# Performance work log

Measured on AMD Instinct MI355X. Metric: run time of the kernel, lower is better.

Reference implementation:

```python
import jax, jax.numpy as jnp
import numpy as np

B, G, D, E = 16, 2048, 2048, 32          # batch, genes, drug fp dim, gene embed dim
NL, NM, H, GS = 16, 4, 6, 64             # n leaves, n mids, term hidden, genes per leaf
GAMMA, NDRUG, EPS = 0.5, 1024, 1e-5

def _bn3(x):  # BatchNorm1d on [B, C, L], training stats, affine at init (gamma=1, beta=0)
    m = x.mean(axis=(0, 2), keepdims=True)
    v = x.var(axis=(0, 2), keepdims=True)
    return (x - m) / jnp.sqrt(v + EPS)

def _bn2(x):  # BatchNorm1d on [B, C]
    m = x.mean(axis=0, keepdims=True)
    v = x.var(axis=0, keepdims=True)
    return (x - m) / jnp.sqrt(v + EPS)

def _term(ci, W1, b1, Wc, bc, Wd, bd):
    # ci: [B, E, in] child input; returns ([B,H,E] 3d out, [B,H] 2d out)
    h = jnp.einsum('bei,hi->bhe', ci, W1) + b1[None, :, None]      # linear -> permute
    h = _bn3(h)
    c = jnp.einsum('bhe,kh->bke', h, Wc) + bc[None, :, None]       # context layer
    out3d = _bn3(c)                                                # [B,H,E]
    mean = out3d.mean(axis=1)                                      # [B,E]
    out2d = _bn2(jnp.tanh(mean @ Wd.T + bd))                       # dimension layer
    return out3d, out2d

def setup_inputs():
    key = jax.random.key(0)
    ks = iter(jax.random.split(key, 64))
    def rn(shape):
        return jax.random.normal(next(ks), shape, dtype=jnp.float32) * 0.05
    x = jax.random.normal(next(ks), (B, G + D + 1), dtype=jnp.float32)
    idx = jax.random.randint(next(ks), (B,), 0, NDRUG)
    x = x.at[:, -1].set(idx.astype(jnp.float32))
    table = jax.random.randint(next(ks), (NDRUG, G), 0, G, dtype=jnp.int32)
    inp = dict(x=x, table=table,
        W_rbf=rn((E, G)), b_rbf=rn((E,)), emb=rn((G, E)),
        W_dg=rn((NL, GS, G)), b_dg=rn((NL, GS)),
        Wl1=rn((NL, H, GS)), bl1=rn((NL, H)), Wlc=rn((NL, H, H)), blc=rn((NL, H)),
        Wld=rn((NL, H, E)), bld=rn((NL, H)),
        Wm1=rn((NM, H, 4 * H)), bm1=rn((NM, H)), Wmc=rn((NM, H, H)), bmc=rn((NM, H)),
        Wmd=rn((NM, H, E)), bmd=rn((NM, H)),
        Wr1=rn((H, 4 * H)), br1=rn((H,)), Wrc=rn((H, H)), brc=rn((H,)),
        Wrd=rn((H, E)), brd=rn((H,)),
        Wd1=rn((100, D)), bd1=rn((100,)), Wd2=rn((50, 100)), bd2=rn((50,)),
        Wd3=rn((H, 50)), bd3=rn((H,)),
        Wf=rn((6, 2 * H)), bf=rn((6,)), Wfa=rn((1, 6)), bfa=rn((1,)),
        Wfo=rn((1, 1)), bfo=rn((1,)))
    return inp

def reference(x, W_rbf, b_rbf, emb, W_dg, b_dg,
              Wl1, bl1, Wlc, blc, Wld, bld,
              Wm1, bm1, Wmc, bmc, Wmd, bmd,
              Wr1, br1, Wrc, brc, Wrd, brd,
              Wd1, bd1, Wd2, bd2, Wd3, bd3,
              Wf, bf, Wfa, bfa, Wfo, bfo, table):
    g = x[:, :G]
    drug = x[:, G:G + D]
    idx = x[:, G + D].astype(jnp.int32)
    # RBF kernel: [B, G, G]
    vect = jnp.exp(-GAMMA * jnp.square(g[:, :, None] - g[:, None, :]))
    gv = jnp.einsum('bij,ej->bie', vect, W_rbf) + b_rbf            # [B,G,E]
    lv = emb[table[idx]]                                            # [B,G,E]
    gf = (gv + lv).transpose(0, 2, 1)                               # [B,E,G]
    # per-leaf direct gene layers
    gene_out = jnp.einsum('beg,lkg->lbek', gf, W_dg) + b_dg[:, None, None, :]  # [NL,B,E,GS]
    leaf3d, _ = jax.vmap(_term)(gene_out, Wl1, bl1, Wlc, blc, Wld, bld)        # [NL,B,H,E]
    # mid terms: concat 4 leaf children along feature dim
    a = leaf3d.transpose(0, 1, 3, 2).reshape(NM, 4, B, E, H)
    a = jnp.moveaxis(a, 1, 3).reshape(NM, B, E, 4 * H)
    mid3d, _ = jax.vmap(_term)(a, Wm1, bm1, Wmc, bmc, Wmd, bmd)                # [NM,B,H,E]
    r = jnp.moveaxis(mid3d.transpose(0, 1, 3, 2), 0, 2).reshape(B, E, 4 * H)
    _, root2d = _term(r, Wr1, br1, Wrc, brc, Wrd, brd)                          # [B,H]
    # drug MLP
    d = drug
    for Wl, bl in ((Wd1, bd1), (Wd2, bd2), (Wd3, bd3)):
        d = _bn2(jnp.tanh(d @ Wl.T + bl))
    fin = jnp.concatenate([root2d, d], axis=1)                                  # [B,2H]
    out = _bn2(jnp.tanh(fin @ Wf.T + bf))
    aux = jnp.tanh(out @ Wfa.T + bfa)
    return aux @ Wfo.T + bfo                                                    # [B,1]
```

## Files before the change

kernel.cpp:

```cpp
#include <hip/hip_runtime.h>
#include <hip/hip_bf16.h>

#define Bb 16
#define Gg 2048
#define Dd 2048
#define XS 4097
#define EPSf 1e-5f
#define CEXP (-0.72134752044448170368f)

typedef unsigned int u32;
typedef __attribute__((ext_vector_type(8))) short bf16x8;
typedef __attribute__((ext_vector_type(4))) float f32x4;

union U16 { uint4 u; bf16x8 v; };

__device__ inline float fast_exp2(float x) {
#if __has_builtin(__builtin_amdgcn_exp2f)
  return __builtin_amdgcn_exp2f(x);
#else
  return exp2f(x);
#endif
}

__device__ inline u32 pk2(float a, float b) {
  return __builtin_amdgcn_perm(__float_as_uint(b), __float_as_uint(a), 0x07060302u);
}
__device__ inline float bftrunc(float a) {
  return __uint_as_float(__float_as_uint(a) & 0xFFFF0000u);
}

__device__ inline void split8(const float* f, U16& hi, U16& lo) {
  u32 h[4], l[4];
  #pragma unroll
  for (int p = 0; p < 4; ++p) {
    float a = f[2 * p], b = f[2 * p + 1];
    h[p] = pk2(a, b);
    l[p] = pk2(a - bftrunc(a), b - bftrunc(b));
  }
  hi.u = make_uint4(h[0], h[1], h[2], h[3]);
  lo.u = make_uint4(l[0], l[1], l[2], l[3]);
}

__device__ inline float wred(float v) {
  #pragma unroll
  for (int o = 32; o > 0; o >>= 1) v += __shfl_xor(v, o, 64);
  return v;
}

__global__ __launch_bounds__(256) void k_split(const float* __restrict__ Wrbf,
                                               const float* __restrict__ Wdg,
                                               u32* __restrict__ Rhi, u32* __restrict__ Rlo,
                                               u32* __restrict__ Dhi, u32* __restrict__ Dlo) {
  int c = blockIdx.x * 256 + threadIdx.x;
  const float* src;
  u32 *dhi, *dlo;
  if (c < 8192) {
    int h = c >> 12, ks = (c >> 6) & 63, l = c & 63;
    src = Wrbf + (h * 16 + (l & 15)) * Gg + ks * 32 + (l >> 4) * 8;
    dhi = Rhi + (size_t)c * 4; dlo = Rlo + (size_t)c * 4;
  } else {
    int cc = c - 8192;
    int nf = cc >> 12, ks = (cc >> 6) & 63, l = cc & 63;
    src = Wdg + (size_t)(nf * 16 + (l & 15)) * Gg + ks * 32 + (l >> 4) * 8;
    dhi = Dhi + (size_t)cc * 4; dlo = Dlo + (size_t)cc * 4;
  }
  float4 f0 = *(const float4*)src;
  float4 f1 = *(const float4*)(src + 4);
  float f[8] = {f0.x, f0.y, f0.z, f0.w, f1.x, f1.y, f1.z, f1.w};
  U16 hi, lo;
  split8(f, hi, lo);
  *(uint4*)dhi = hi.u;
  *(uint4*)dlo = lo.u;
}

__global__ __launch_bounds__(512) void k_rbf(const float* __restrict__ x,
                                             const u32* __restrict__ Whi,
                                             const u32* __restrict__ Wlo,
                                             float4* __restrict__ partR) {
  __shared__ float g_s[512];
  __shared__ u32 w_s[8192];
  const int tid = threadIdx.x;
  const int lane = tid & 63, wid = tid >> 6;
  const int it = blockIdx.x, b = blockIdx.y, jc = blockIdx.z;
  const int i0w = it * 128 + wid * 16;
  g_s[tid] = x[(size_t)b * XS + jc * 512 + tid];
  const float gi = x[(size_t)b * XS + i0w + (lane & 15)];
  f32x4 acc0 = {0.f, 0.f, 0.f, 0.f};
  f32x4 acc1 = {0.f, 0.f, 0.f, 0.f};
  const int jb = (lane >> 4) * 8;
  const int ksbase = jc * 16;

  uint4 pf[4];
  #pragma unroll
  for (int sg = 0; sg < 4; ++sg) {
    int seg = wid * 4 + sg;
    int arr = seg >> 4, h = (seg >> 3) & 1, ksl = seg & 7;
    pf[sg] = *(const uint4*)((arr ? Wlo : Whi) +
             (((size_t)h * 64 + ksbase + ksl) * 64 + lane) * 4);
  }
  for (int chunk = 0; chunk < 2; ++chunk) {
    __syncthreads();
    #pragma unroll
    for (int sg = 0; sg < 4; ++sg)
      *(uint4*)&w_s[(wid * 4 + sg) * 256 + lane * 4] = pf[sg];
    if (chunk < 1) {
      #pragma unroll
      for (int sg = 0; sg < 4; ++sg) {
        int seg = wid * 4 + sg;
        int arr = seg >> 4, h = (seg >> 3) & 1, ksl = seg & 7;
        pf[sg] = *(const uint4*)((arr ? Wlo : Whi) +
                 (((size_t)h * 64 + ksbase + 8 + ksl) * 64 + lane) * 4);
      }
    }
    __syncthreads();
    #pragma unroll
    for (int ksl = 0; ksl < 8; ++ksl) {
      const float* gp = &g_s[chunk * 256 + ksl * 32 + jb];
      float4 gja = *(const float4*)gp;
      float4 gjb = *(const float4*)(gp + 4);
      float gv[8] = {gja.x, gja.y, gja.z, gja.w, gjb.x, gjb.y, gjb.z, gjb.w};
      float kv[8];
      #pragma unroll
      for (int q = 0; q < 8; ++q) {
        float d = gi - gv[q];
        kv[q] = fast_exp2(d * d * CEXP);
      }
      U16 ah, al;
      split8(kv, ah, al);
      U16 w0h, w1h, w0l, w1l;
      w0h.u = *(const uint4*)&w_s[(ksl) * 256 + lane * 4];
      w1h.u = *(const uint4*)&w_s[(8 + ksl) * 256 + lane * 4];
      w0l.u = *(const uint4*)&w_s[(16 + ksl) * 256 + lane * 4];
      w1l.u = *(const uint4*)&w_s[(24 + ksl) * 256 + lane * 4];
      acc0 = __builtin_amdgcn_mfma_f32_16x16x32_bf16(ah.v, w0h.v, acc0, 0, 0, 0);
      acc0 = __builtin_amdgcn_mfma_f32_16x16x32_bf16(al.v, w0h.v, acc0, 0, 0, 0);
      acc0 = __builtin_amdgcn_mfma_f32_16x16x32_bf16(ah.v, w0l.v, acc0, 0, 0, 0);
      acc1 = __builtin_amdgcn_mfma_f32_16x16x32_bf16(ah.v, w1h.v, acc1, 0, 0, 0);
      acc1 = __builtin_amdgcn_mfma_f32_16x16x32_bf16(al.v, w1h.v, acc1, 0, 0, 0);
      acc1 = __builtin_amdgcn_mfma_f32_16x16x32_bf16(ah.v, w1l.v, acc1, 0, 0, 0);
    }
  }
  size_t pbase = (((((size_t)jc * 16 + b) * 16 + it) * 8 + wid) * 2) * 64 + lane;
  partR[pbase]      = make_float4(acc0[0], acc0[1], acc0[2], acc0[3]);
  partR[pbase + 64] = make_float4(acc1[0], acc1[1], acc1[2], acc1[3]);
}

__global__ __launch_bounds__(256) void k_pack(const float4* __restrict__ partR,
                                              const float* __restrict__ x,
                                              const int* __restrict__ table,
                                              const float* __restrict__ emb,
                                              const float* __restrict__ brbf,
                                              u32* __restrict__ Ahi,
                                              u32* __restrict__ Alo) {
  int u = blockIdx.x * 256 + threadIdx.x;
  int lane = u & 63, hb = (u >> 6) & 1, wid = (u >> 7) & 7;
  int it = (u >> 10) & 15, b = u >> 14;
  float4 p0 = partR[u];
  float4 p1 = partR[262144 + u];
  float4 p2 = partR[524288 + u];
  float4 p3 = partR[786432 + u];
  int eloc = lane & 15, quad = lane >> 4;
  int e = hb * 16 + eloc;
  int i0w = it * 128 + wid * 16;
  int ib = i0w + quad * 4;
  int idx = (int)x[(size_t)b * XS + Gg + Dd];
  int4 tt = *(const int4*)&table[(size_t)idx * Gg + ib];
  float bias = brbf[e];
  float v0 = p0.x + p1.x + p2.x + p3.x + bias + emb[tt.x * 32 + e];
  float v1 = p0.y + p1.y + p2.y + p3.y + bias + emb[tt.y * 32 + e];
  float v2 = p0.z + p1.z + p2.z + p3.z + bias + emb[tt.z * 32 + e];
  float v3 = p0.w + p1.w + p2.w + p3.w + bias + emb[tt.w * 32 + e];
  int ks = i0w >> 5;
  int lp = (2 * ((i0w >> 4) & 1) + (quad >> 1)) * 16 + eloc;
  int hs = quad & 1;
  size_t off = (((size_t)(b * 2 + hb) * 64 + ks) * 64 + lp) * 4 + hs * 2;
  Ahi[off]     = pk2(v0, v1);
  Ahi[off + 1] = pk2(v2, v3);
  Alo[off]     = pk2(v0 - bftrunc(v0), v1 - bftrunc(v1));
  Alo[off + 1] = pk2(v2 - bftrunc(v2), v3 - bftrunc(v3));
}

__global__ __launch_bounds__(512) void k_mm(const u32* __restrict__ Ahi,
                                            const u32* __restrict__ Alo,
                                            const u32* __restrict__ Bhi,
                                            const u32* __restrict__ Blo,
                                            float* __restrict__ part) {
  __shared__ u32 s_mm[6144];
  const int tid = threadIdx.x;
  const int lane = tid & 63, wid = tid >> 6;
  const int id = blockIdx.x;
  const int pl = id & 7, by = (id >> 3) & 7, ph = id >> 6;
  const int p = ph * 8 + pl;
  const int bx = p >> 2, kc = p & 3;
  const int wm = wid >> 2, wn = wid & 3;
  f32x4 acc[2][2];
  #pragma unroll
  for (int mf = 0; mf < 2; ++mf)
    #pragma unroll
    for (int nf = 0; nf < 2; ++nf) acc[mf][nf] = (f32x4){0.f, 0.f, 0.f, 0.f};

  uint4 pf[3];
  #pragma unroll
  for (int q = 0; q < 3; ++q) {
    int seg = wid * 3 + q;
    const u32* src;
    if (seg < 8) {
      int hl = seg >> 2, mf = seg & 3;
      src = (hl ? Alo : Ahi) + (((size_t)(by * 4 + mf) * 64 + kc * 16) * 64 + lane) * 4;
    } else {
      int t = seg - 8, hl = t >> 3, nf = t & 7;
      src = (hl ? Blo : Bhi) + (((size_t)(bx * 8 + nf) * 64 + kc * 16) * 64 + lane) * 4;
    }
    pf[q] = *(const uint4*)src;
  }
  for (int stage = 0; stage < 16; ++stage) {
    __syncthreads();
    #pragma unroll
    for (int q = 0; q < 3; ++q)
      *(uint4*)&s_mm[(wid * 3 + q) * 256 + lane * 4] = pf[q];
    if (stage < 15) {
      const int ks = kc * 16 + stage + 1;
      #pragma unroll
      for (int q = 0; q < 3; ++q) {
        int seg = wid * 3 + q;
        const u32* src;
        if (seg < 8) {
          int hl = seg >> 2, mf = seg & 3;
          src = (hl ? Alo : Ahi) + (((size_t)(by * 4 + mf) * 64 + ks) * 64 + lane) * 4;
        } else {
          int t = seg - 8, hl = t >> 3, nf = t & 7;
          src = (hl ? Blo : Bhi) + (((size_t)(bx * 8 + nf) * 64 + ks) * 64 + lane) * 4;
        }
        pf[q] = *(const uint4*)src;
      }
    }
    __syncthreads();
    U16 ah[2], al[2], bh[2], bl[2];
    #pragma unroll
    for (int mf = 0; mf < 2; ++mf) {
      ah[mf].u = *(const uint4*)&s_mm[(0 + wm * 2 + mf) * 256 + lane * 4];
      al[mf].u = *(const uint4*)&s_mm[(4 + wm * 2 + mf) * 256 + lane * 4];
    }
    #pragma unroll
    for (int nf = 0; nf < 2; ++nf) {
      bh[nf].u = *(const uint4*)&s_mm[(8 + wn * 2 + nf) * 256 + lane * 4];
      bl[nf].u = *(const uint4*)&s_mm[(16 + wn * 2 + nf) * 256 + lane * 4];
    }
    #pragma unroll
    for (int mf = 0; mf < 2; ++mf) {
      #pragma unroll
      for (int nf = 0; nf < 2; ++nf) {
        acc[mf][nf] = __builtin_amdgcn_mfma_f32_16x16x32_bf16(ah[mf].v, bh[nf].v, acc[mf][nf], 0, 0, 0);
        acc[mf][nf] = __builtin_amdgcn_mfma_f32_16x16x32_bf16(al[mf].v, bh[nf].v, acc[mf][nf], 0, 0, 0);
        acc[mf][nf] = __builtin_amdgcn_mfma_f32_16x16x32_bf16(ah[mf].v, bl[nf].v, acc[mf][nf], 0, 0, 0);
      }
    }
  }
  const int quad = lane >> 4, nl = lane & 15;
  #pragma unroll
  for (int mf = 0; mf < 2; ++mf) {
    #pragma unroll
    for (int nf = 0; nf < 2; ++nf) {
      int n  = bx * 128 + wn * 32 + nf * 16 + nl;
      int m0 = by * 64 + wm * 32 + mf * 16 + quad * 4;
      float4 st = make_float4(acc[mf][nf][0], acc[mf][nf][1], acc[mf][nf][2], acc[mf][nf][3]);
      *(float4*)&part[(size_t)kc * 524288 + (size_t)n * 512 + m0] = st;
    }
  }
}

__device__ inline void bn512(float* v, int wv, int lane,
                             float (*r1)[6], float (*r2)[6]) {
  float s[6], q[6];
  #pragma unroll
  for (int c = 0; c < 6; ++c) {
    float a = v[c];
    s[c] = wred(a);
    q[c] = wred(a * a);
  }
  __syncthreads();
  if (lane == 0) {
    #pragma unroll
    for (int c = 0; c < 6; ++c) { r1[wv][c] = s[c]; r2[wv][c] = q[c]; }
  }
  __syncthreads();
  #pragma unroll
  for (int c = 0; c < 6; ++c) {
    float S = 0.f, Q = 0.f;
    #pragma unroll
    for (int w = 0; w < 8; ++w) { S += r1[w][c]; Q += r2[w][c]; }
    float m  = S * (1.0f / 512.0f);
    float va = Q * (1.0f / 512.0f) - m * m;
    v[c] = (v[c] - m) * rsqrtf(va + EPSf);
  }
}

__global__ __launch_bounds__(512) void k_leaf(const float* __restrict__ part,
                                              const float* __restrict__ bdg,
                                              const float* __restrict__ W1,
                                              const float* __restrict__ b1,
                                              const float* __restrict__ Wc,
                                              const float* __restrict__ bc,
                                              float* __restrict__ outp) {
  const int l = blockIdx.x, tid = threadIdx.x;
  const int wv = tid >> 6, lane = tid & 63;
  __shared__ float r1[8][6], r2[8][6];
  float cv[64];
  #pragma unroll
  for (int i = 0; i < 64; ++i) {
    int n = l * 64 + i;
    const float* pp = part + (size_t)n * 512 + tid;
    cv[i] = pp[0] + pp[524288] + pp[2 * 524288] + pp[3 * 524288] + bdg[n];
  }
  const float* w1 = W1 + l * 6 * 64;
  float h[6];
  #pragma unroll
  for (int hh = 0; hh < 6; ++hh) {
    float s = b1[l * 6 + hh];
    #pragma unroll
    for (int i = 0; i < 64; ++i) s = fmaf(cv[i], w1[hh * 64 + i], s);
    h[hh] = s;
  }
  bn512(h, wv, lane, r1, r2);
  float c[6];
  #pragma unroll
  for (int k = 0; k < 6; ++k) {
    float s = bc[l * 6 + k];
    #pragma unroll
    for (int hh = 0; hh < 6; ++hh) s = fmaf(h[hh], Wc[l * 36 + k * 6 + hh], s);
    c[k] = s;
  }
  bn512(c, wv, lane, r1, r2);
  float* o = outp + (((size_t)(l >> 2) * 512 + tid) * 24 + (l & 3) * 6);
  #pragma unroll
  for (int k = 0; k < 6; ++k) o[k] = c[k];
}

__global__ __launch_bounds__(512) void k_mid(const float* __restrict__ gin,
                                             const float* __restrict__ W1,
                                             const float* __restrict__ b1,
                                             const float* __restrict__ Wc,
                                             const float* __restrict__ bc,
                                             float* __restrict__ outp) {
  const int l = blockIdx.x, tid = threadIdx.x;
  const int wv = tid >> 6, lane = tid & 63;
  __shared__ float r1[8][6], r2[8][6];
  const float* ci = gin + ((size_t)l * 512 + tid) * 24;
  float cv[24];
  #pragma unroll
  for (int q = 0; q < 6; ++q) *(float4*)&cv[q * 4] = ((const float4*)ci)[q];
  const float* w1 = W1 + l * 6 * 24;
  float h[6];
  #pragma unroll
  for (int hh = 0; hh < 6; ++hh) {
    float s = b1[l * 6 + hh];
    #pragma unroll
    for (int i = 0; i < 24; ++i) s = fmaf(cv[i], w1[hh * 24 + i], s);
    h[hh] = s;
  }
  bn512(h, wv, lane, r1, r2);
  float c[6];
  #pragma unroll
  for (int k = 0; k < 6; ++k) {
    float s = bc[l * 6 + k];
    #pragma unroll
    for (int hh = 0; hh < 6; ++hh) s = fmaf(h[hh], Wc[l * 36 + k * 6 + hh], s);
    c[k] = s;
  }
  bn512(c, wv, lane, r1, r2);
  float* o = outp + ((size_t)tid * 24 + l * 6);
  #pragma unroll
  for (int k = 0; k < 6; ++k) o[k] = c[k];
}

__global__ __launch_bounds__(1024) void k_drug1(const float* __restrict__ x,
                                                const float* __restrict__ Wd1,
                                                const float* __restrict__ bd1,
                                                float* __restrict__ d1) {
  const int c = blockIdx.x;
  const int tid = threadIdx.x;
  const int b = tid >> 6, lane = tid & 63;
  const float* xb = x + (size_t)b * XS + Gg;
  const float* w = Wd1 + (size_t)c * 2048;
  float s = 0.f;
  #pragma unroll
  for (int q = 0; q < 8; ++q) {
    int k = q * 256 + lane * 4;
    float4 xv = *(const float4*)(xb + k);
    float4 wv = *(const float4*)(w + k);
    s = fmaf(xv.x, wv.x, s);
    s = fmaf(xv.y, wv.y, s);
    s = fmaf(xv.z, wv.z, s);
    s = fmaf(xv.w, wv.w, s);
  }
  s = wred(s);
  __shared__ float y[16];
  if (lane == 0) y[b] = tanhf(s + bd1[c]);
  __syncthreads();
  if (tid < 16) {
    float S = 0.f, Q = 0.f;
    #pragma unroll
    for (int bb = 0; bb < 16; ++bb) { float v = y[bb]; S += v; Q += v * v; }
    float m = S * (1.0f / 16.0f), va = Q * (1.0f / 16.0f) - m * m;
    d1[tid * 100 + c] = (y[tid] - m) * rsqrtf(va + EPSf);
  }
}

__global__ __launch_bounds__(512) void k_rootfinal(const float* __restrict__ rootin,
                                                   const float* __restrict__ d1,
                                                   const float* __restrict__ Wr1,
                                                   const float* __restrict__ br1,
                                                   const float* __restrict__ Wrc,
                                                   const float* __restrict__ brc,
                                                   const float* __restrict__ Wrd,
                                                   const float* __restrict__ brd,
                                                   const float* __restrict__ Wd2,
                                                   const float* __restrict__ bd2,
                                                   const float* __restrict__ Wd3,
                                                   const float* __restrict__ bd3,
                                                   const float* __restrict__ Wf,
                                                   const float* __restrict__ bf,
                                                   const float* __restrict__ Wfa,
                                                   const float* __restrict__ bfa,
                                                   const float* __restrict__ Wfo,
                                                   const float* __restrict__ bfo,
                                                   float* __restrict__ out) {
  const int tid = threadIdx.x;
  const int wv = tid >> 6, lane = tid & 63;
  __shared__ float r1[8][6], r2[8][6];
  __shared__ float w2s[50 * 101];
  __shared__ float d1s[1600];
  __shared__ float r2ds[96];
  for (int u = tid; u < 5000; u += 512) w2s[(u / 100) * 101 + (u % 100)] = Wd2[u];
  for (int u = tid; u < 1600; u += 512) d1s[u] = d1[u];

  const float* ci = rootin + (size_t)tid * 24;
  float cv[24];
  #pragma unroll
  for (int q = 0; q < 6; ++q) *(float4*)&cv[q * 4] = ((const float4*)ci)[q];
  float h[6];
  #pragma unroll
  for (int hh = 0; hh < 6; ++hh) {
    float s = br1[hh];
    #pragma unroll
    for (int i = 0; i < 24; ++i) s = fmaf(cv[i], Wr1[hh * 24 + i], s);
    h[hh] = s;
  }
  bn512(h, wv, lane, r1, r2);
  float c[6];
  #pragma unroll
  for (int k = 0; k < 6; ++k) {
    float s = brc[k];
    #pragma unroll
    for (int hh = 0; hh < 6; ++hh) s = fmaf(h[hh], Wrc[k * 6 + hh], s);
    c[k] = s;
  }
  bn512(c, wv, lane, r1, r2);
  float mv = (c[0] + c[1] + c[2] + c[3] + c[4] + c[5]) * (1.0f / 6.0f);
  __shared__ float shm[512];
  shm[tid] = mv;
  __syncthreads();
  __shared__ float st[96];
  if (tid < 96) {
    int b = tid / 6, hh = tid % 6;
    float s = brd[hh];
    #pragma unroll
    for (int e = 0; e < 32; ++e) s = fmaf(shm[b * 32 + e], Wrd[hh * 32 + e], s);
    st[tid] = tanhf(s);
  }
  __syncthreads();
  if (tid < 6) {
    float S = 0.f, Q = 0.f;
    for (int b = 0; b < 16; ++b) { float v = st[b * 6 + tid]; S += v; Q += v * v; }
    float m = S * (1.0f / 16.0f), va = Q * (1.0f / 16.0f) - m * m;
    float iv = rsqrtf(va + EPSf);
    for (int b = 0; b < 16; ++b) r2ds[b * 6 + tid] = (st[b * 6 + tid] - m) * iv;
  }
  __syncthreads();

  __shared__ float s2[800], mu2[50], iv2[50];
  for (int u = tid; u < 800; u += 512) {
    int b = u / 50, cc = u % 50;
    float s = bd2[cc];
    #pragma unroll
    for (int k = 0; k < 100; ++k) s = fmaf(d1s[b * 100 + k], w2s[cc * 101 + k], s);
    s2[u] = tanhf(s);
  }
  __syncthreads();
  if (tid < 50) {
    float S = 0.f, Q = 0.f;
    #pragma unroll
    for (int b = 0; b < 16; ++b) { float v = s2[b * 50 + tid]; S += v; Q += v * v; }
    float m = S * (1.0f / 16.0f), va = Q * (1.0f / 16.0f) - m * m;
    mu2[tid] = m; iv2[tid] = rsqrtf(va + EPSf);
  }
  __syncthreads();
  __shared__ float s3[96], mu3[6], iv3[6];
  if (tid < 96) {
    int b = tid / 6, cc = tid % 6;
    float s = bd3[cc];
    #pragma unroll
    for (int k = 0; k < 50; ++k)
      s = fmaf((s2[b * 50 + k] - mu2[k]) * iv2[k], Wd3[cc * 50 + k], s);
    s3[tid] = tanhf(s);
  }
  __syncthreads();
  if (tid < 6) {
    float S = 0.f, Q = 0.f;
    #pragma unroll
    for (int b = 0; b < 16; ++b) { float v = s3[b * 6 + tid]; S += v; Q += v * v; }
    float m = S * (1.0f / 16.0f), va = Q * (1.0f / 16.0f) - m * m;
    mu3[tid] = m; iv3[tid] = rsqrtf(va + EPSf);
  }
  __syncthreads();
  __shared__ float sf[96], muf[6], ivf[6];
  if (tid < 96) {
    int b = tid / 6, cc = tid % 6;
    float s = bf[cc];
    #pragma unroll
    for (int q = 0; q < 6; ++q) s = fmaf(r2ds[b * 6 + q], Wf[cc * 12 + q], s);
    #pragma unroll
    for (int q = 0; q < 6; ++q)
      s = fmaf((s3[b * 6 + q] - mu3[q]) * iv3[q], Wf[cc * 12 + 6 + q], s);
    sf[tid] = tanhf(s);
  }
  __syncthreads();
  if (tid < 6) {
    float S = 0.f, Q = 0.f;
    #pragma unroll
    for (int b = 0; b < 16; ++b) { float v = sf[b * 6 + tid]; S += v; Q += v * v; }
    float m = S * (1.0f / 16.0f), va = Q * (1.0f / 16.0f) - m * m;
    muf[tid] = m; ivf[tid] = rsqrtf(va + EPSf);
  }
  __syncthreads();
  if (tid < 16) {
    float s = bfa[0];
    #pragma unroll
    for (int q = 0; q < 6; ++q)
      s = fmaf((sf[tid * 6 + q] - muf[q]) * ivf[q], Wfa[q], s);
    float a = tanhf(s);
    out[tid] = a * Wfo[0] + bfo[0];
  }
}

extern "C" void kernel_launch(void* const* d_in, const int* in_sizes, int n_in,
                              void* d_out, int out_size, void* d_ws, size_t ws_size,
                              hipStream_t stream) {
  const float* x     = (const float*)d_in[0];
  const int*   table = (const int*)d_in[1];
  const float* Wrbf  = (const float*)d_in[2];
  const float* brbf  = (const float*)d_in[3];
  const float* emb   = (const float*)d_in[4];
  const float* Wdg   = (const float*)d_in[5];
  const float* bdg   = (const float*)d_in[6];
  const float* Wl1   = (const float*)d_in[7];
  const float* bl1   = (const float*)d_in[8];
  const float* Wlc   = (const float*)d_in[9];
  const float* blc   = (const float*)d_in[10];
  const float* Wm1   = (const float*)d_in[13];
  const float* bm1   = (const float*)d_in[14];
  const float* Wmc   = (const float*)d_in[15];
  const float* bmc   = (const float*)d_in[16];
  const float* Wr1   = (const float*)d_in[19];
  const float* br1   = (const float*)d_in[20];
  const float* Wrc   = (const float*)d_in[21];
  const float* brc   = (const float*)d_in[22];
  const float* Wrd   = (const float*)d_in[23];
  const float* brd   = (const float*)d_in[24];
  const float* Wd1   = (const float*)d_in[25];
  const float* bd1   = (const float*)d_in[26];
  const float* Wd2   = (const float*)d_in[27];
  const float* bd2   = (const float*)d_in[28];
  const float* Wd3   = (const float*)d_in[29];
  const float* bd3   = (const float*)d_in[30];
  const float* Wf    = (const float*)d_in[31];
  const float* bf    = (const float*)d_in[32];
  const float* Wfa   = (const float*)d_in[33];
  const float* bfa   = (const float*)d_in[34];
  const float* Wfo   = (const float*)d_in[35];
  const float* bfo   = (const float*)d_in[36];
  float* out = (float*)d_out;

  u32* Rhi = (u32*)d_ws;
  u32* Rlo = Rhi + 32768;
  u32* Dhi = Rlo + 32768;
  u32* Dlo = Dhi + 1048576;
  u32* Ahi = Dlo + 1048576;
  u32* Alo = Ahi + 524288;
  float4* partR = (float4*)(Alo + 524288);
  float* partB = (float*)(partR + 1048576);
  float* midin = partB + 4 * 524288;
  float* rootin= midin + 49152;
  float* d1    = rootin + 12288;

  hipLaunchKernelGGL(k_drug1,     dim3(100),       dim3(1024), 0, stream, x, Wd1, bd1, d1);
  hipLaunchKernelGGL(k_split,     dim3(1056),      dim3(256),  0, stream, Wrbf, Wdg, Rhi, Rlo, Dhi, Dlo);
  hipLaunchKernelGGL(k_rbf,       dim3(16, 16, 4), dim3(512),  0, stream, x, Rhi, Rlo, partR);
  hipLaunchKernelGGL(k_pack,      dim3(1024),      dim3(256),  0, stream, partR, x, table, emb, brbf, Ahi, Alo);
  hipLaunchKernelGGL(k_mm,        dim3(256),       dim3(512),  0, stream, Ahi, Alo, Dhi, Dlo, partB);
  hipLaunchKernelGGL(k_leaf,      dim3(16),        dim3(512),  0, stream, partB, bdg, Wl1, bl1, Wlc, blc, midin);
  hipLaunchKernelGGL(k_mid,       dim3(4),         dim3(512),  0, stream, midin, Wm1, bm1, Wmc, bmc, rootin);
  hipLaunchKernelGGL(k_rootfinal, dim3(1),         dim3(512),  0, stream, rootin, d1,
                     Wr1, br1, Wrc, brc, Wrd, brd, Wd2, bd2, Wd3, bd3,
                     Wf, bf, Wfa, bfa, Wfo, bfo, out);
}
```

Measured before the change: 126.3 us.

## Fuse RBF kernel and pack step with in-block split-K reduction

Merges k_rbf and k_pack into one kernel. Each 1024-thread block now covers all four K-chunks for 64 genes and reduces the partial sums through shared memory. The float4 partial-sum buffer, its global round trip and one launch go away. Weights are now read straight from global memory (cache) instead of being staged in shared memory, and only a quarter of the warps do the final pack. Fewer blocks (512 instead of 1024) may reduce latency hiding.

```diff
diff --git a/kernel.cpp b/kernel.cpp
--- a/kernel.cpp
+++ b/kernel.cpp
@@ -73,111 +73,88 @@
   *(uint4*)dlo = lo.u;
 }
 
-__global__ __launch_bounds__(512) void k_rbf(const float* __restrict__ x,
-                                             const u32* __restrict__ Whi,
-                                             const u32* __restrict__ Wlo,
-                                             float4* __restrict__ partR) {
-  __shared__ float g_s[512];
-  __shared__ u32 w_s[8192];
+__global__ __launch_bounds__(1024) void k_rbf2(const float* __restrict__ x,
+                                               const u32* __restrict__ Whi,
+                                               const u32* __restrict__ Wlo,
+                                               const int* __restrict__ table,
+                                               const float* __restrict__ emb,
+                                               const float* __restrict__ brbf,
+                                               u32* __restrict__ Ahi,
+                                               u32* __restrict__ Alo) {
+  __shared__ float g_s[2048];
+  __shared__ float red[16][64][8];
   const int tid = threadIdx.x;
   const int lane = tid & 63, wid = tid >> 6;
-  const int it = blockIdx.x, b = blockIdx.y, jc = blockIdx.z;
-  const int i0w = it * 128 + wid * 16;
-  g_s[tid] = x[(size_t)b * XS + jc * 512 + tid];
+  const int isub = wid >> 2, jcw = wid & 3;
+  const int i0 = blockIdx.x * 64, b = blockIdx.y;
+  const int i0w = i0 + isub * 16;
+  g_s[tid] = x[(size_t)b * XS + tid];
+  g_s[tid + 1024] = x[(size_t)b * XS + 1024 + tid];
   const float gi = x[(size_t)b * XS + i0w + (lane & 15)];
   f32x4 acc0 = {0.f, 0.f, 0.f, 0.f};
   f32x4 acc1 = {0.f, 0.f, 0.f, 0.f};
   const int jb = (lane >> 4) * 8;
-  const int ksbase = jc * 16;
-
-  uint4 pf[4];
-  #pragma unroll
-  for (int sg = 0; sg < 4; ++sg) {
-    int seg = wid * 4 + sg;
-    int arr = seg >> 4, h = (seg >> 3) & 1, ksl = seg & 7;
-    pf[sg] = *(const uint4*)((arr ? Wlo : Whi) +
-             (((size_t)h * 64 + ksbase + ksl) * 64 + lane) * 4);
-  }
-  for (int chunk = 0; chunk < 2; ++chunk) {
-    __syncthreads();
-    #pragma unroll
-    for (int sg = 0; sg < 4; ++sg)
-      *(uint4*)&w_s[(wid * 4 + sg) * 256 + lane * 4] = pf[sg];
-    if (chunk < 1) {
-      #pragma unroll
-      for (int sg = 0; sg < 4; ++sg) {
-        int seg = wid * 4 + sg;
-        int arr = seg >> 4, h = (seg >> 3) & 1, ksl = seg & 7;
-        pf[sg] = *(const uint4*)((arr ? Wlo : Whi) +
-                 (((size_t)h * 64 + ksbase + 8 + ksl) * 64 + lane) * 4);
-      }
-    }
-    __syncthreads();
-    #pragma unroll
-    for (int ksl = 0; ksl < 8; ++ksl) {
-      const float* gp = &g_s[chunk * 256 + ksl * 32 + jb];
-      float4 gja = *(const float4*)gp;
-      float4 gjb = *(const float4*)(gp + 4);
-      float gv[8] = {gja.x, gja.y, gja.z, gja.w, gjb.x, gjb.y, gjb.z, gjb.w};
-      float kv[8];
-      #pragma unroll
-      for (int q = 0; q < 8; ++q) {
-        float d = gi - gv[q];
-        kv[q] = fast_exp2(d * d * CEXP);
-      }
-      U16 ah, al;
-      split8(kv, ah, al);
-      U16 w0h, w1h, w0l, w1l;
-      w0h.u = *(const uint4*)&w_s[(ksl) * 256 + lane * 4];
-      w1h.u = *(const uint4*)&w_s[(8 + ksl) * 256 + lane * 4];
-      w0l.u = *(const uint4*)&w_s[(16 + ksl) * 256 + lane * 4];
-      w1l.u = *(const uint4*)&w_s[(24 + ksl) * 256 + lane * 4];
-      acc0 = __builtin_amdgcn_mfma_f32_16x16x32_bf16(ah.v, w0h.v, acc0, 0, 0, 0);
-      acc0 = __builtin_amdgcn_mfma_f32_16x16x32_bf16(al.v, w0h.v, acc0, 0, 0, 0);
-      acc0 = __builtin_amdgcn_mfma_f32_16x16x32_bf16(ah.v, w0l.v, acc0, 0, 0, 0);
-      acc1 = __builtin_amdgcn_mfma_f32_16x16x32_bf16(ah.v, w1h.v, acc1, 0, 0, 0);
-      acc1 = __builtin_amdgcn_mfma_f32_16x16x32_bf16(al.v, w1h.v, acc1, 0, 0, 0);
-      acc1 = __builtin_amdgcn_mfma_f32_16x16x32_bf16(ah.v, w1l.v, acc1, 0, 0, 0);
-    }
-  }
-  size_t pbase = (((((size_t)jc * 16 + b) * 16 + it) * 8 + wid) * 2) * 64 + lane;
-  partR[pbase]      = make_float4(acc0[0], acc0[1], acc0[2], acc0[3]);
-  partR[pbase + 64] = make_float4(acc1[0], acc1[1], acc1[2], acc1[3]);
-}
-
-__global__ __launch_bounds__(256) void k_pack(const float4* __restrict__ partR,
-                                              const float* __restrict__ x,
-                                              const int* __restrict__ table,
-                                              const float* __restrict__ emb,
-                                              const float* __restrict__ brbf,
-                                              u32* __restrict__ Ahi,
-                                              u32* __restrict__ Alo) {
-  int u = blockIdx.x * 256 + threadIdx.x;
-  int lane = u & 63, hb = (u >> 6) & 1, wid = (u >> 7) & 7;
-  int it = (u >> 10) & 15, b = u >> 14;
-  float4 p0 = partR[u];
-  float4 p1 = partR[262144 + u];
-  float4 p2 = partR[524288 + u];
-  float4 p3 = partR[786432 + u];
-  int eloc = lane & 15, quad = lane >> 4;
-  int e = hb * 16 + eloc;
-  int i0w = it * 128 + wid * 16;
-  int ib = i0w + quad * 4;
-  int idx = (int)x[(size_t)b * XS + Gg + Dd];
-  int4 tt = *(const int4*)&table[(size_t)idx * Gg + ib];
-  float bias = brbf[e];
-  float v0 = p0.x + p1.x + p2.x + p3.x + bias + emb[tt.x * 32 + e];
-  float v1 = p0.y + p1.y + p2.y + p3.y + bias + emb[tt.y * 32 + e];
-  float v2 = p0.z + p1.z + p2.z + p3.z + bias + emb[tt.z * 32 + e];
-  float v3 = p0.w + p1.w + p2.w + p3.w + bias + emb[tt.w * 32 + e];
-  int ks = i0w >> 5;
-  int lp = (2 * ((i0w >> 4) & 1) + (quad >> 1)) * 16 + eloc;
-  int hs = quad & 1;
-  size_t off = (((size_t)(b * 2 + hb) * 64 + ks) * 64 + lp) * 4 + hs * 2;
-  Ahi[off]     = pk2(v0, v1);
-  Ahi[off + 1] = pk2(v2, v3);
-  Alo[off]     = pk2(v0 - bftrunc(v0), v1 - bftrunc(v1));
-  Alo[off + 1] = pk2(v2 - bftrunc(v2), v3 - bftrunc(v3));
+  __syncthreads();
+
+  #pragma unroll
+  for (int ksl = 0; ksl < 16; ++ksl) {
+    const int ks = jcw * 16 + ksl;
+    const float* gp = &g_s[ks * 32 + jb];
+    float4 gja = *(const float4*)gp;
+    float4 gjb = *(const float4*)(gp + 4);
+    float gv[8] = {gja.x, gja.y, gja.z, gja.w, gjb.x, gjb.y, gjb.z, gjb.w};
+    float kv[8];
+    #pragma unroll
+    for (int q = 0; q < 8; ++q) {
+      float d = gi - gv[q];
+      kv[q] = fast_exp2(d * d * CEXP);
+    }
+    U16 ah, al;
+    split8(kv, ah, al);
+    U16 w0h, w1h, w0l, w1l;
+    const size_t wo = (size_t)ks * 256 + lane * 4;
+    w0h.u = *(const uint4*)(Whi + wo);
+    w1h.u = *(const uint4*)(Whi + 16384 + wo);
+    w0l.u = *(const uint4*)(Wlo + wo);
+    w1l.u = *(const uint4*)(Wlo + 16384 + wo);
+    acc0 = __builtin_amdgcn_mfma_f32_16x16x32_bf16(ah.v, w0h.v, acc0, 0, 0, 0);
+    acc0 = __builtin_amdgcn_mfma_f32_16x16x32_bf16(al.v, w0h.v, acc0, 0, 0, 0);
+    acc0 = __builtin_amdgcn_mfma_f32_16x16x32_bf16(ah.v, w0l.v, acc0, 0, 0, 0);
+    acc1 = __builtin_amdgcn_mfma_f32_16x16x32_bf16(ah.v, w1h.v, acc1, 0, 0, 0);
+    acc1 = __builtin_amdgcn_mfma_f32_16x16x32_bf16(al.v, w1h.v, acc1, 0, 0, 0);
+    acc1 = __builtin_amdgcn_mfma_f32_16x16x32_bf16(ah.v, w1l.v, acc1, 0, 0, 0);
+  }
+  #pragma unroll
+  for (int k = 0; k < 4; ++k) { red[wid][lane][k] = acc0[k]; red[wid][lane][4 + k] = acc1[k]; }
+  __syncthreads();
+  if (jcw == 0) {
+    float f[8];
+    #pragma unroll
+    for (int k = 0; k < 8; ++k)
+      f[k] = red[isub * 4][lane][k] + red[isub * 4 + 1][lane][k] +
+             red[isub * 4 + 2][lane][k] + red[isub * 4 + 3][lane][k];
+    const int idx = (int)x[(size_t)b * XS + Gg + Dd];
+    const int eloc = lane & 15, quad = lane >> 4;
+    const int ib = i0w + quad * 4;
+    int4 tt = *(const int4*)&table[(size_t)idx * Gg + ib];
+    const int ks = i0w >> 5;
+    const int lp = (2 * ((i0w >> 4) & 1) + (quad >> 1)) * 16 + eloc;
+    const int hs = quad & 1;
+    #pragma unroll
+    for (int hb = 0; hb < 2; ++hb) {
+      const int e = hb * 16 + eloc;
+      const float bias = brbf[e];
+      float v0 = f[hb * 4 + 0] + bias + emb[tt.x * 32 + e];
+      float v1 = f[hb * 4 + 1] + bias + emb[tt.y * 32 + e];
+      float v2 = f[hb * 4 + 2] + bias + emb[tt.z * 32 + e];
+      float v3 = f[hb * 4 + 3] + bias + emb[tt.w * 32 + e];
+      size_t off = (((size_t)(b * 2 + hb) * 64 + ks) * 64 + lp) * 4 + hs * 2;
+      Ahi[off]     = pk2(v0, v1);
+      Ahi[off + 1] = pk2(v2, v3);
+      Alo[off]     = pk2(v0 - bftrunc(v0), v1 - bftrunc(v1));
+      Alo[off + 1] = pk2(v2 - bftrunc(v2), v3 - bftrunc(v3));
+    }
+  }
 }
 
 __global__ __launch_bounds__(512) void k_mm(const u32* __restrict__ Ahi,
@@ -587,20 +564,18 @@
   u32* Dlo = Dhi + 1048576;
   u32* Ahi = Dlo + 1048576;
   u32* Alo = Ahi + 524288;
-  float4* partR = (float4*)(Alo + 524288);
-  float* partB = (float*)(partR + 1048576);
+  float* partB = (float*)(Alo + 524288);
   float* midin = partB + 4 * 524288;
   float* rootin= midin + 49152;
   float* d1    = rootin + 12288;
 
-  hipLaunchKernelGGL(k_drug1,     dim3(100),       dim3(1024), 0, stream, x, Wd1, bd1, d1);
-  hipLaunchKernelGGL(k_split,     dim3(1056),      dim3(256),  0, stream, Wrbf, Wdg, Rhi, Rlo, Dhi, Dlo);
-  hipLaunchKernelGGL(k_rbf,       dim3(16, 16, 4), dim3(512),  0, stream, x, Rhi, Rlo, partR);
-  hipLaunchKernelGGL(k_pack,      dim3(1024),      dim3(256),  0, stream, partR, x, table, emb, brbf, Ahi, Alo);
-  hipLaunchKernelGGL(k_mm,        dim3(256),       dim3(512),  0, stream, Ahi, Alo, Dhi, Dlo, partB);
-  hipLaunchKernelGGL(k_leaf,      dim3(16),        dim3(512),  0, stream, partB, bdg, Wl1, bl1, Wlc, blc, midin);
-  hipLaunchKernelGGL(k_mid,       dim3(4),         dim3(512),  0, stream, midin, Wm1, bm1, Wmc, bmc, rootin);
-  hipLaunchKernelGGL(k_rootfinal, dim3(1),         dim3(512),  0, stream, rootin, d1,
+  hipLaunchKernelGGL(k_drug1,     dim3(100),    dim3(1024), 0, stream, x, Wd1, bd1, d1);
+  hipLaunchKernelGGL(k_split,     dim3(1056),   dim3(256),  0, stream, Wrbf, Wdg, Rhi, Rlo, Dhi, Dlo);
+  hipLaunchKernelGGL(k_rbf2,      dim3(32, 16), dim3(1024), 0, stream, x, Rhi, Rlo, table, emb, brbf, Ahi, Alo);
+  hipLaunchKernelGGL(k_mm,        dim3(256),    dim3(512),  0, stream, Ahi, Alo, Dhi, Dlo, partB);
+  hipLaunchKernelGGL(k_leaf,      dim3(16),     dim3(512),  0, stream, partB, bdg, Wl1, bl1, Wlc, blc, midin);
+  hipLaunchKernelGGL(k_mid,       dim3(4),      dim3(512),  0, stream, midin, Wm1, bm1, Wmc, bmc, rootin);
+  hipLaunchKernelGGL(k_rootfinal, dim3(1),      dim3(512),  0, stream, rootin, d1,
                      Wr1, br1, Wrc, brc, Wrd, brd, Wd2, bd2, Wd3, bd3,
                      Wf, bf, Wfa, bfa, Wfo, bfo, out);
 }
```

Result: faster. 115.6 us (-8.5%).
